# Performance work log

Measured on AMD Instinct MI355X. Metric: run time of the kernel, lower is better.

The kernel has to match this reference:

```python
import jax, jax.numpy as jnp
import numpy as np

N_VOCAB = 50257
N_EMBED = 300
N_HIDDEN = 256
N_OUTPUT = 1
BATCH = 256
SEQ_LEN = 512


def setup_inputs() -> dict:
    key = jax.random.key(0)
    k1, k2, k3, k4, k5, k6 = jax.random.split(key, 6)
    input_words = jax.random.randint(k1, (BATCH, SEQ_LEN), 0, N_VOCAB, dtype=jnp.int64 if jax.config.jax_enable_x64 else jnp.int32)
    emb_table = jax.random.normal(k2, (N_VOCAB, N_EMBED), dtype=jnp.float32)
    Wi = jax.random.normal(k3, (N_EMBED, N_HIDDEN), dtype=jnp.float32)
    Wh = jax.random.normal(k4, (N_HIDDEN, N_HIDDEN), dtype=jnp.float32)
    # nn.Linear default init: U(-1/sqrt(in), 1/sqrt(in))
    bound = 1.0 / np.sqrt(N_HIDDEN)
    fc_w = jax.random.uniform(k5, (N_HIDDEN, N_OUTPUT), minval=-bound, maxval=bound, dtype=jnp.float32)
    fc_b = jax.random.uniform(k6, (N_OUTPUT,), minval=-bound, maxval=bound, dtype=jnp.float32)
    return {"input_words": input_words, "emb_table": emb_table, "Wi": Wi, "Wh": Wh, "fc_w": fc_w, "fc_b": fc_b}


def reference(input_words, emb_table, Wi, Wh, fc_w, fc_b):
    # [B, S, E] -> [S, B, E] (module permutes to time-major)
    embedded = emb_table[input_words].transpose(1, 0, 2)
    h0 = jnp.zeros((input_words.shape[0], Wh.shape[0]), dtype=embedded.dtype)

    def step(h, x_t):
        # recurrence: h = sigmoid(x_t @ Wi + h @ Wh)
        h_new = jax.nn.sigmoid(x_t @ Wi + h @ Wh)
        return h_new, None

    hidden, _ = jax.lax.scan(step, h0, embedded)
    sig = jax.nn.sigmoid(hidden @ fc_w + fc_b)
    return (sig, hidden)
```

## Files before the change

kernel.cpp:

```cpp
#include <hip/hip_runtime.h>

#define S_LEN 512
#define BATCH 256
#define EMB   300
#define HID   256
#define VOCAB 50257
#define NPROD 786
#define NLOG2E -1.44269504089f

#define EW_BYTES 25731584ull
#define KPAD 320

typedef __attribute__((ext_vector_type(8))) _Float16 f16x8;
typedef __attribute__((ext_vector_type(4))) _Float16 f16x4;
typedef __attribute__((ext_vector_type(2))) __fp16   fp16v2;
typedef __attribute__((ext_vector_type(4))) float    f32x4;

__device__ __forceinline__ void block_sync_lds() {
    asm volatile("" ::: "memory");
    __builtin_amdgcn_s_waitcnt(0xC07F);
    __builtin_amdgcn_s_barrier();
    asm volatile("" ::: "memory");
}

__device__ __forceinline__ float sigmoid_scaled(float xs) {
    float e = __builtin_amdgcn_exp2f(xs);
    return __builtin_amdgcn_rcpf(1.0f + e);
}

__global__ __launch_bounds__(256)
void k_wprep(const float* __restrict__ Wi, _Float16* __restrict__ WiT) {
    const int k = blockIdx.x;
    const int n = threadIdx.x;
    _Float16 v = (_Float16)0.f;
    if (k < EMB) v = (_Float16)(Wi[k * HID + n] * NLOG2E);
    WiT[n * KPAD + k] = v;
}

__global__ __launch_bounds__(256, 3)
void k_embwi(const float* __restrict__ emb, const _Float16* __restrict__ WiT,
             _Float16* __restrict__ EW) {
    const int tid  = threadIdx.x;
    const int wv   = tid >> 6;
    const int lane = tid & 63;
    const int ln   = lane & 15;
    const int q    = lane >> 4;
    const int m0   = blockIdx.x * 64;

    const _Float16* wbn[4];
#pragma unroll
    for (int nt = 0; nt < 4; nt++)
        wbn[nt] = WiT + (wv * 64 + nt * 16 + ln) * KPAD + q * 8;

    const float* arow[4];
#pragma unroll
    for (int mt = 0; mt < 4; mt++) {
        int row = m0 + mt * 16 + ln; if (row >= VOCAB) row = VOCAB - 1;
        arow[mt] = emb + (long)row * EMB + q * 8;
    }

    auto load_af = [&](int kc, int mt) -> f16x8 {
        const float* p = arow[mt] + kc * 32;
        f16x8 v;
        if (kc < 9 || q == 0) {
            f32x4 a = *(const f32x4*)p;
            f32x4 b = *(const f32x4*)(p + 4);
#pragma unroll
            for (int r = 0; r < 4; r++) { v[r] = (_Float16)a[r]; v[4 + r] = (_Float16)b[r]; }
        } else if (q == 1) {
            f32x4 a = *(const f32x4*)p;
#pragma unroll
            for (int r = 0; r < 4; r++) { v[r] = (_Float16)a[r]; v[4 + r] = (_Float16)0.f; }
        } else {
#pragma unroll
            for (int r = 0; r < 8; r++) v[r] = (_Float16)0.f;
        }
        return v;
    };

    f32x4 acc[4][4];
#pragma unroll
    for (int mt = 0; mt < 4; mt++)
#pragma unroll
        for (int nt = 0; nt < 4; nt++)
            acc[mt][nt] = f32x4{0.f, 0.f, 0.f, 0.f};

#pragma unroll
    for (int kc = 0; kc < 10; kc++) {
        f16x8 af[4], bf[4];
#pragma unroll
        for (int mt = 0; mt < 4; mt++) af[mt] = load_af(kc, mt);
#pragma unroll
        for (int nt = 0; nt < 4; nt++) bf[nt] = *(const f16x8*)(wbn[nt] + kc * 32);
#pragma unroll
        for (int mt = 0; mt < 4; mt++)
#pragma unroll
            for (int nt = 0; nt < 4; nt++)
                acc[mt][nt] = __builtin_amdgcn_mfma_f32_16x16x32_f16(
                    af[mt], bf[nt], acc[mt][nt], 0, 0, 0);
    }

#pragma unroll
    for (int mt = 0; mt < 4; mt++)
#pragma unroll
        for (int nt = 0; nt < 4; nt++) {
            const int col = wv * 64 + nt * 16 + ln;
#pragma unroll
            for (int r = 0; r < 4; r++) {
                const int mm = m0 + mt * 16 + q * 4 + r;
                if (mm < VOCAB) EW[(long)mm * HID + col] = (_Float16)acc[mt][nt][r];
            }
        }
}

#define HSTR 264
#define HB8  (8 * HSTR)
#define WSTR 513

__global__ __launch_bounds__(512, 2)
void k_recur(const float* __restrict__ Wh, const _Float16* __restrict__ EW,
             const int* __restrict__ words,
             const float* __restrict__ fcw, const float* __restrict__ fcb,
             float* __restrict__ out) {
    __shared__ __attribute__((aligned(16))) _Float16 hbuf[2 * HB8];
    __shared__ float red[512];
    __shared__ int   wlds[8 * WSTR];

    const int tid  = threadIdx.x;
    const int wv   = tid >> 6;
    const int lane = tid & 63;
    const int ln   = lane & 15;
    const int lnn  = ln & 7;
    const int q    = lane >> 4;
    const int b0   = blockIdx.x * 8;

    f16x8 whf[8][2];
#pragma unroll
    for (int kc = 0; kc < 8; kc++) {
#pragma unroll
        for (int mt = 0; mt < 2; mt++) {
            const int j = wv * 32 + mt * 16 + ln;
            f16x8 u;
#pragma unroll
            for (int jj = 0; jj < 8; jj++)
                u[jj] = (_Float16)(Wh[(kc * 32 + q * 8 + jj) * HID + j] * NLOG2E);
            whf[kc][mt] = u;
        }
    }

#pragma unroll
    for (int i = tid; i < 8 * S_LEN; i += 512) {
        const int r = i >> 9, c = i & 511;
        wlds[r * WSTR + c] = words[(b0 + r) * S_LEN + c];
    }
    for (int i = tid; i < 2 * HB8; i += 512) hbuf[i] = (_Float16)0.f;
    __syncthreads();

    const int jbase = wv * 32 + q * 4;
    f16x4 abuf0[2], abuf1[2];
    {
        const int w0 = wlds[lnn * WSTR + 0];
        const int w1 = wlds[lnn * WSTR + 1];
        const _Float16* p0 = EW + ((long)w0 << 8) + jbase;
        const _Float16* p1 = EW + ((long)w1 << 8) + jbase;
#pragma unroll
        for (int mt = 0; mt < 2; mt++) abuf0[mt] = *(const f16x4*)(p0 + mt * 16);
#pragma unroll
        for (int mt = 0; mt < 2; mt++) abuf1[mt] = *(const f16x4*)(p1 + mt * 16);
    }

#define STEP(T, ABUF)                                                                   \
    {                                                                                   \
        const int tt = (T);                                                             \
        const _Float16* hr = hbuf + ((tt & 1) ? HB8 : 0);                               \
        _Float16*       hw = hbuf + ((tt & 1) ? 0 : HB8);                               \
        f16x8 hf[8];                                                                    \
        _Pragma("unroll")                                                               \
        for (int kc = 0; kc < 8; kc++)                                                  \
            hf[kc] = *(const f16x8*)(hr + lnn * HSTR + kc * 32 + q * 8);                \
        f32x4 acc_a[2], acc_b[2];                                                       \
        _Pragma("unroll")                                                               \
        for (int mt = 0; mt < 2; mt++) {               \
            f16x4 av = ABUF[mt];                                                        \
            acc_a[mt] = f32x4{(float)av[0], (float)av[1], (float)av[2], (float)av[3]};  \
            acc_b[mt] = f32x4{0.f, 0.f, 0.f, 0.f};                                      \
        }                                                                               \
        const int t2 = (tt + 2 > 511) ? 511 : (tt + 2);                                 \
        const int wrow = wlds[lnn * WSTR + t2];                                         \
        const _Float16* rp = EW + ((long)wrow << 8) + jbase;                            \
        _Pragma("unroll")                                                               \
        for (int mt = 0; mt < 2; mt++) ABUF[mt] = *(const f16x4*)(rp + mt * 16);        \
        _Pragma("unroll")                                                               \
        for (int r = 0; r < 4; r++) {                            \
            _Pragma("unroll")                                                           \
            for (int mt = 0; mt < 2; mt++)                                              \
                acc_a[mt] = __builtin_amdgcn_mfma_f32_16x16x32_f16(                     \
                    whf[r][mt], hf[r], acc_a[mt], 0, 0, 0);                             \
            _Pragma("unroll")                                                           \
            for (int mt = 0; mt < 2; mt++)                                              \
                acc_b[mt] = __builtin_amdgcn_mfma_f32_16x16x32_f16(                     \
                    whf[r + 4][mt], hf[r + 4], acc_b[mt], 0, 0, 0);                     \
        }                                                                               \
        _Pragma("unroll")                                                               \
        for (int mt = 0; mt < 2; mt++) {                                                \
            f32x4 s = acc_a[mt] + acc_b[mt];                                            \
            float r0 = sigmoid_scaled(s[0]), r1 = sigmoid_scaled(s[1]);                 \
            float r2 = sigmoid_scaled(s[2]), r3 = sigmoid_scaled(s[3]);                 \
            union { fp16v2 h2[2]; f16x4 v4; } hp;                                       \
            hp.h2[0] = __builtin_amdgcn_cvt_pkrtz(r0, r1);                              \
            hp.h2[1] = __builtin_amdgcn_cvt_pkrtz(r2, r3);                              \
            if (ln < 8)                                                                 \
                *(f16x4*)(hw + ln * HSTR + wv * 32 + mt * 16 + q * 4) = hp.v4;          \
        }                                                                               \
        block_sync_lds();                                                               \
    }

    for (int t = 0; t < S_LEN; t += 2) {
        STEP(t, abuf0);
        STEP(t + 1, abuf1);
    }
#undef STEP

    const _Float16* hf0 = hbuf;

    {
        const int row = tid >> 6, j0 = (tid & 63) * 4;
        float* dst = out + 256 + (long)(b0 + row) * HID + j0;
        f32x4 w;
#pragma unroll
        for (int r = 0; r < 4; r++) w[r] = (float)hf0[row * HSTR + j0 + r];
        *(f32x4*)dst = w;
    }

    {
        const int row = tid >> 6, part = tid & 63;
        float s = 0.f;
#pragma unroll
        for (int jj = 0; jj < 4; jj++) {
            const int j = part * 4 + jj;
            s += (float)hf0[row * HSTR + j] * fcw[j];
        }
        red[row * 64 + part] = s;
    }
    __syncthreads();
    if (tid < 8) {
        float s = fcb[0];
#pragma unroll
        for (int p = 0; p < 64; p++) s += red[tid * 64 + p];
        s *= NLOG2E;
        out[b0 + tid] = sigmoid_scaled(s);
    }
}

extern "C" void kernel_launch(void* const* d_in, const int* in_sizes, int n_in,
                              void* d_out, int out_size, void* d_ws, size_t ws_size,
                              hipStream_t stream) {
    const int*   words = (const int*)d_in[0];
    const float* emb   = (const float*)d_in[1];
    const float* Wi    = (const float*)d_in[2];
    const float* Wh    = (const float*)d_in[3];
    const float* fcw   = (const float*)d_in[4];
    const float* fcb   = (const float*)d_in[5];
    _Float16* EW   = (_Float16*)d_ws;
    _Float16* WiT  = (_Float16*)((char*)d_ws + EW_BYTES);
    float*    outp = (float*)d_out;

    hipLaunchKernelGGL(k_wprep, dim3(KPAD), dim3(256), 0, stream, Wi, WiT);
    hipLaunchKernelGGL(k_embwi, dim3(NPROD), dim3(256), 0, stream, emb, WiT, EW);
    hipLaunchKernelGGL(k_recur, dim3(BATCH / 8), dim3(512), 0, stream,
                       Wh, EW, words, fcw, fcb, outp);
}
```

Baseline: 422.0 us.

## Split recurrent hidden dimension across 16 waves per block instead of 8

The recurrence kernel now launches 1024 threads per block. Each of the 16 waves owns 16 hidden columns instead of 32, so each wave issues 8 MFMAs per step instead of 16 and keeps half as many Wh fragments in registers. The hidden-state LDS row stride also changes from 264 to 272, which alters the LDS bank pattern. The intent is to shorten the serial per-step critical path by spreading the MFMA work over more waves, at the cost of a barrier across 16 waves each step and one block per CU.

```diff
diff --git a/kernel.cpp b/kernel.cpp
--- a/kernel.cpp
+++ b/kernel.cpp
@@ -113,11 +113,11 @@
         }
 }
 
-#define HSTR 264
+#define HSTR 272
 #define HB8  (8 * HSTR)
 #define WSTR 513
 
-__global__ __launch_bounds__(512, 2)
+__global__ __launch_bounds__(1024, 1)
 void k_recur(const float* __restrict__ Wh, const _Float16* __restrict__ EW,
              const int* __restrict__ words,
              const float* __restrict__ fcw, const float* __restrict__ fcb,
@@ -134,39 +134,32 @@
     const int q    = lane >> 4;
     const int b0   = blockIdx.x * 8;
 
-    f16x8 whf[8][2];
+    f16x8 whf[8];
 #pragma unroll
     for (int kc = 0; kc < 8; kc++) {
-#pragma unroll
-        for (int mt = 0; mt < 2; mt++) {
-            const int j = wv * 32 + mt * 16 + ln;
-            f16x8 u;
-#pragma unroll
-            for (int jj = 0; jj < 8; jj++)
-                u[jj] = (_Float16)(Wh[(kc * 32 + q * 8 + jj) * HID + j] * NLOG2E);
-            whf[kc][mt] = u;
-        }
-    }
-
-#pragma unroll
-    for (int i = tid; i < 8 * S_LEN; i += 512) {
+        const int j = wv * 16 + ln;
+        f16x8 u;
+#pragma unroll
+        for (int jj = 0; jj < 8; jj++)
+            u[jj] = (_Float16)(Wh[(kc * 32 + q * 8 + jj) * HID + j] * NLOG2E);
+        whf[kc] = u;
+    }
+
+#pragma unroll
+    for (int i = tid; i < 8 * S_LEN; i += 1024) {
         const int r = i >> 9, c = i & 511;
         wlds[r * WSTR + c] = words[(b0 + r) * S_LEN + c];
     }
-    for (int i = tid; i < 2 * HB8; i += 512) hbuf[i] = (_Float16)0.f;
+    for (int i = tid; i < 2 * HB8; i += 1024) hbuf[i] = (_Float16)0.f;
     __syncthreads();
 
-    const int jbase = wv * 32 + q * 4;
-    f16x4 abuf0[2], abuf1[2];
+    const int jbase = wv * 16 + q * 4;
+    f16x4 abuf0, abuf1;
     {
         const int w0 = wlds[lnn * WSTR + 0];
         const int w1 = wlds[lnn * WSTR + 1];
-        const _Float16* p0 = EW + ((long)w0 << 8) + jbase;
-        const _Float16* p1 = EW + ((long)w1 << 8) + jbase;
-#pragma unroll
-        for (int mt = 0; mt < 2; mt++) abuf0[mt] = *(const f16x4*)(p0 + mt * 16);
-#pragma unroll
-        for (int mt = 0; mt < 2; mt++) abuf1[mt] = *(const f16x4*)(p1 + mt * 16);
+        abuf0 = *(const f16x4*)(EW + ((long)w0 << 8) + jbase);
+        abuf1 = *(const f16x4*)(EW + ((long)w1 << 8) + jbase);
     }
 
 #define STEP(T, ABUF)                                                                   \
@@ -178,39 +171,31 @@
         _Pragma("unroll")                                                               \
         for (int kc = 0; kc < 8; kc++)                                                  \
             hf[kc] = *(const f16x8*)(hr + lnn * HSTR + kc * 32 + q * 8);                \
-        f32x4 acc_a[2], acc_b[2];                                                       \
-        _Pragma("unroll")                                                               \
-        for (int mt = 0; mt < 2; mt++) {               \
-            f16x4 av = ABUF[mt];                                                        \
-            acc_a[mt] = f32x4{(float)av[0], (float)av[1], (float)av[2], (float)av[3]};  \
-            acc_b[mt] = f32x4{0.f, 0.f, 0.f, 0.f};                                      \
+        f32x4 acc_a, acc_b;                                                             \
+        {                                              \
+            f16x4 av = ABUF;                                                            \
+            acc_a = f32x4{(float)av[0], (float)av[1], (float)av[2], (float)av[3]};      \
+            acc_b = f32x4{0.f, 0.f, 0.f, 0.f};                                          \
         }                                                                               \
         const int t2 = (tt + 2 > 511) ? 511 : (tt + 2);                                 \
         const int wrow = wlds[lnn * WSTR + t2];                                         \
-        const _Float16* rp = EW + ((long)wrow << 8) + jbase;                            \
-        _Pragma("unroll")                                                               \
-        for (int mt = 0; mt < 2; mt++) ABUF[mt] = *(const f16x4*)(rp + mt * 16);        \
+        ABUF = *(const f16x4*)(EW + ((long)wrow << 8) + jbase);                         \
         _Pragma("unroll")                                                               \
         for (int r = 0; r < 4; r++) {                            \
-            _Pragma("unroll")                                                           \
-            for (int mt = 0; mt < 2; mt++)                                              \
-                acc_a[mt] = __builtin_amdgcn_mfma_f32_16x16x32_f16(                     \
-                    whf[r][mt], hf[r], acc_a[mt], 0, 0, 0);                             \
-            _Pragma("unroll")                                                           \
-            for (int mt = 0; mt < 2; mt++)                                              \
-                acc_b[mt] = __builtin_amdgcn_mfma_f32_16x16x32_f16(                     \
-                    whf[r + 4][mt], hf[r + 4], acc_b[mt], 0, 0, 0);                     \
+            acc_a = __builtin_amdgcn_mfma_f32_16x16x32_f16(                             \
+                whf[r], hf[r], acc_a, 0, 0, 0);                                         \
+            acc_b = __builtin_amdgcn_mfma_f32_16x16x32_f16(                             \
+                whf[r + 4], hf[r + 4], acc_b, 0, 0, 0);                                 \
         }                                                                               \
-        _Pragma("unroll")                                                               \
-        for (int mt = 0; mt < 2; mt++) {                                                \
-            f32x4 s = acc_a[mt] + acc_b[mt];                                            \
+        {                                                                               \
+            f32x4 s = acc_a + acc_b;                                                    \
             float r0 = sigmoid_scaled(s[0]), r1 = sigmoid_scaled(s[1]);                 \
             float r2 = sigmoid_scaled(s[2]), r3 = sigmoid_scaled(s[3]);                 \
             union { fp16v2 h2[2]; f16x4 v4; } hp;                                       \
             hp.h2[0] = __builtin_amdgcn_cvt_pkrtz(r0, r1);                              \
             hp.h2[1] = __builtin_amdgcn_cvt_pkrtz(r2, r3);                              \
             if (ln < 8)                                                                 \
-                *(f16x4*)(hw + ln * HSTR + wv * 32 + mt * 16 + q * 4) = hp.v4;          \
+                *(f16x4*)(hw + ln * HSTR + wv * 16 + q * 4) = hp.v4;                    \
         }                                                                               \
         block_sync_lds();                                                               \
     }
@@ -223,7 +208,7 @@
 
     const _Float16* hf0 = hbuf;
 
-    {
+    if (tid < 512) {
         const int row = tid >> 6, j0 = (tid & 63) * 4;
         float* dst = out + 256 + (long)(b0 + row) * HID + j0;
         f32x4 w;
@@ -232,7 +217,7 @@
         *(f32x4*)dst = w;
     }
 
-    {
+    if (tid < 512) {
         const int row = tid >> 6, part = tid & 63;
         float s = 0.f;
 #pragma unroll
@@ -267,6 +252,6 @@
 
     hipLaunchKernelGGL(k_wprep, dim3(KPAD), dim3(256), 0, stream, Wi, WiT);
     hipLaunchKernelGGL(k_embwi, dim3(NPROD), dim3(256), 0, stream, emb, WiT, EW);
-    hipLaunchKernelGGL(k_recur, dim3(BATCH / 8), dim3(512), 0, stream,
+    hipLaunchKernelGGL(k_recur, dim3(BATCH / 8), dim3(1024), 0, stream,
                        Wh, EW, words, fcw, fcb, outp);
 }
```

Result: no change. 420.2 us (-0.4%).
